# Performance work log

Hardware: AMD Instinct MI355X
Metric: run time of the kernel (lower is better)

## Reference

```python
import jax, jax.numpy as jnp
import numpy as np


def setup_inputs() -> dict:
    key = jax.random.key(0)
    k1, k2 = jax.random.split(key)
    B, W, F = 8, 4096, 64
    subed = jax.random.normal(k1, (B, W, F), dtype=jnp.float32)
    sub = jax.random.normal(k2, (B, W, F), dtype=jnp.float32)
    return {"subed": subed, "sub": sub, "d": 8}


def reference(subed, sub, d):
    # subed, sub: [B, W, F]
    W = subed.shape[1]
    # delays = [0, 1..d, -1..-d]; torch pads sub with W copies of first/last row,
    # then gathers at index W + t + delay, which equals sub[clip(t+delay, 0, W-1)].
    delays = jnp.concatenate(
        [jnp.zeros((1,), jnp.int32), jnp.arange(1, d + 1, dtype=jnp.int32), -jnp.arange(1, d + 1, dtype=jnp.int32)]
    )  # [K] with K = 2d+1
    idx = jnp.clip(jnp.arange(W, dtype=jnp.int32)[:, None] + delays[None, :], 0, W - 1)  # [W, K]
    gathered = sub[:, idx, :]  # [B, W, K, F]
    res = subed[:, :, None, :] - gathered  # [B, W, K, F]
    k = jnp.argmin(jnp.abs(res), axis=2)  # [B, W, F] (first min on ties, as torch)
    out = jnp.take_along_axis(res, k[:, :, None, :], axis=2)[:, :, 0, :]  # [B, W, F]
    return out
```

## Files before the change

### kernel.cpp

```cpp
#include <hip/hip_runtime.h>


#define B_DIM 8
#define W_DIM 4096
#define F_DIM 64
#define FVEC  (F_DIM / 4)

__global__ __launch_bounds__(256) void offsub_kernel(
    const float4* __restrict__ subed,
    const float4* __restrict__ sub,
    const int* __restrict__ d_ptr,
    float4* __restrict__ out)
{
    const int tid = blockIdx.x * blockDim.x + threadIdx.x;
    const int total = B_DIM * W_DIM * FVEC;
    if (tid >= total) return;

    const int d = *d_ptr;

    const int fv = tid & (FVEC - 1);
    const int bw = tid / FVEC;
    const int w  = bw & (W_DIM - 1);
    const int b  = bw / W_DIM;

    const size_t rowBase = (size_t)b * W_DIM * FVEC + fv;

    const float4 s = subed[tid];

    float4 g = sub[rowBase + (size_t)w * FVEC];
    float rx = s.x - g.x, ry = s.y - g.y, rz = s.z - g.z, rw = s.w - g.w;
    float ax = fabsf(rx), ay = fabsf(ry), az = fabsf(rz), aw = fabsf(rw);
    float bx = rx, by = ry, bz = rz, bww = rw;

    for (int pass = 0; pass < 2; ++pass) {
        for (int dlt = 1; dlt <= d; ++dlt) {
            int wi = (pass == 0) ? min(w + dlt, W_DIM - 1) : max(w - dlt, 0);
            g = sub[rowBase + (size_t)wi * FVEC];
            float tx = s.x - g.x, ty = s.y - g.y, tz = s.z - g.z, tw = s.w - g.w;
            float cx = fabsf(tx), cy = fabsf(ty), cz = fabsf(tz), cw = fabsf(tw);
            if (cx < ax) { ax = cx; bx = tx; }
            if (cy < ay) { ay = cy; by = ty; }
            if (cz < az) { az = cz; bz = tz; }
            if (cw < aw) { aw = cw; bww = tw; }
        }
    }

    float4 o; o.x = bx; o.y = by; o.z = bz; o.w = bww;
    out[tid] = o;
}

extern "C" void kernel_launch(void* const* d_in, const int* in_sizes, int n_in,
                              void* d_out, int out_size, void* d_ws, size_t ws_size,
                              hipStream_t stream)
{
    const float4* subed = (const float4*)d_in[0];
    const float4* sub   = (const float4*)d_in[1];
    const int*    dptr  = (const int*)d_in[2];
    float4* out = (float4*)d_out;

    const int total  = B_DIM * W_DIM * FVEC;
    const int block  = 256;
    const int grid   = (total + block - 1) / block;

    offsub_kernel<<<grid, block, 0, stream>>>(subed, sub, dptr, out);
}
```

Before: 13.16 us.

## Process two rows per thread with fully unrolled window loads for d==8

Each thread now handles two adjacent W rows and, on a fast path specialized for d==8, loads the 18 shared sub rows into registers once, reusing them for both outputs. The fully unrolled gather replaces the data-dependent loop, exposing all loads at once for memory-level parallelism. A generic fallback path keeps other d values correct. The cost is higher register pressure and half as many threads, which lowers occupancy.

```diff
diff --git a/kernel.cpp b/kernel.cpp
--- a/kernel.cpp
+++ b/kernel.cpp
@@ -3,8 +3,22 @@
 
 #define B_DIM 8
 #define W_DIM 4096
-#define F_DIM 64
-#define FVEC  (F_DIM / 4)
+#define FVEC  16
+#define RW    2
+#define WP    (W_DIM / RW)
+#define LOG2_WP 11
+
+__device__ __forceinline__ float4 f4sub(float4 a, float4 b) {
+    float4 r; r.x = a.x - b.x; r.y = a.y - b.y; r.z = a.z - b.z; r.w = a.w - b.w;
+    return r;
+}
+
+__device__ __forceinline__ void upd(float4& best, float4 cand) {
+    best.x = (fabsf(cand.x) < fabsf(best.x)) ? cand.x : best.x;
+    best.y = (fabsf(cand.y) < fabsf(best.y)) ? cand.y : best.y;
+    best.z = (fabsf(cand.z) < fabsf(best.z)) ? cand.z : best.z;
+    best.w = (fabsf(cand.w) < fabsf(best.w)) ? cand.w : best.w;
+}
 
 __global__ __launch_bounds__(256) void offsub_kernel(
     const float4* __restrict__ subed,
@@ -13,40 +27,52 @@
     float4* __restrict__ out)
 {
     const int tid = blockIdx.x * blockDim.x + threadIdx.x;
-    const int total = B_DIM * W_DIM * FVEC;
-    if (tid >= total) return;
-
     const int d = *d_ptr;
 
-    const int fv = tid & (FVEC - 1);
-    const int bw = tid / FVEC;
-    const int w  = bw & (W_DIM - 1);
-    const int b  = bw / W_DIM;
+    const int fv   = tid & (FVEC - 1);
+    const int rest = tid >> 4;
+    const int p    = rest & (WP - 1);
+    const int b    = rest >> LOG2_WP;
+    const int w0   = p * RW;
 
-    const size_t rowBase = (size_t)b * W_DIM * FVEC + fv;
+    const size_t base = (size_t)b * (W_DIM * FVEC) + fv;
 
-    const float4 s = subed[tid];
-
-    float4 g = sub[rowBase + (size_t)w * FVEC];
-    float rx = s.x - g.x, ry = s.y - g.y, rz = s.z - g.z, rw = s.w - g.w;
-    float ax = fabsf(rx), ay = fabsf(ry), az = fabsf(rz), aw = fabsf(rw);
-    float bx = rx, by = ry, bz = rz, bww = rw;
-
-    for (int pass = 0; pass < 2; ++pass) {
-        for (int dlt = 1; dlt <= d; ++dlt) {
-            int wi = (pass == 0) ? min(w + dlt, W_DIM - 1) : max(w - dlt, 0);
-            g = sub[rowBase + (size_t)wi * FVEC];
-            float tx = s.x - g.x, ty = s.y - g.y, tz = s.z - g.z, tw = s.w - g.w;
-            float cx = fabsf(tx), cy = fabsf(ty), cz = fabsf(tz), cw = fabsf(tw);
-            if (cx < ax) { ax = cx; bx = tx; }
-            if (cy < ay) { ay = cy; by = ty; }
-            if (cz < az) { az = cz; bz = tz; }
-            if (cw < aw) { aw = cw; bww = tw; }
+    if (__builtin_expect(d == 8, 1)) {
+        float4 g[16 + RW];
+        #pragma unroll
+        for (int k = 0; k < 16 + RW; ++k) {
+            int wi = w0 - 8 + k;
+            wi = wi < 0 ? 0 : (wi > W_DIM - 1 ? W_DIM - 1 : wi);
+            g[k] = sub[base + (size_t)wi * FVEC];
+        }
+        #pragma unroll
+        for (int r = 0; r < RW; ++r) {
+            const int w = w0 + r;
+            const float4 s = subed[base + (size_t)w * FVEC];
+            float4 best = f4sub(s, g[r + 8]);
+            #pragma unroll
+            for (int dd = 1; dd <= 8; ++dd)
+                upd(best, f4sub(s, g[r + 8 + dd]));
+            #pragma unroll
+            for (int dd = 1; dd <= 8; ++dd)
+                upd(best, f4sub(s, g[r + 8 - dd]));
+            out[base + (size_t)w * FVEC] = best;
+        }
+    } else {
+        for (int r = 0; r < RW; ++r) {
+            const int w = w0 + r;
+            const float4 s = subed[base + (size_t)w * FVEC];
+            float4 best = f4sub(s, sub[base + (size_t)w * FVEC]);
+            for (int pass = 0; pass < 2; ++pass) {
+                for (int dd = 1; dd <= d; ++dd) {
+                    int wi = (pass == 0) ? min(w + dd, W_DIM - 1)
+                                         : max(w - dd, 0);
+                    upd(best, f4sub(s, sub[base + (size_t)wi * FVEC]));
+                }
+            }
+            out[base + (size_t)w * FVEC] = best;
         }
     }
-
-    float4 o; o.x = bx; o.y = by; o.z = bz; o.w = bww;
-    out[tid] = o;
 }
 
 extern "C" void kernel_launch(void* const* d_in, const int* in_sizes, int n_in,
@@ -58,9 +84,9 @@
     const int*    dptr  = (const int*)d_in[2];
     float4* out = (float4*)d_out;
 
-    const int total  = B_DIM * W_DIM * FVEC;
-    const int block  = 256;
-    const int grid   = (total + block - 1) / block;
+    const int total = B_DIM * WP * FVEC;
+    const int block = 256;
+    const int grid  = (total + block - 1) / block;
 
     offsub_kernel<<<grid, block, 0, stream>>>(subed, sub, dptr, out);
 }
```

Result: faster. 10.85 us (-17.5%).
